# Kernel optimization log

Hardware: AMD Instinct MI355X
Metric: run time of the kernel (lower is better)

The kernel has to match this reference:

```python
import jax, jax.numpy as jnp
import numpy as np

B, N_PER_GRAPH = 16, 512          # uniform graphs -> to_dense_batch is a reshape
N_TOKENS = B * N_PER_GRAPH
M = 32                            # neighbors per node
D_MODEL, D_EDGE, H = 256, 128, 8


def _layernorm(x, g, b, eps=1e-5):
    m = jnp.mean(x, axis=-1, keepdims=True)
    v = jnp.mean((x - m) ** 2, axis=-1, keepdims=True)
    return (x - m) * jax.lax.rsqrt(v + eps) * g + b


def _frame_ops():
    # 2^3 = 8 sign-flip operations, matches FrameAveraging.create_ops
    d = jnp.array([-1.0, 1.0], dtype=jnp.float32)
    g = jnp.meshgrid(d, d, d, indexing='ij')
    return jnp.stack(g, axis=-1).reshape(8, 3)


def _forward(token_embs, geo_feats, edge_feats, neighbor_indices, neighbor_masks,
             ln_qkv_g, ln_qkv_b, W_qkv, b_qkv, ln_e_g, ln_e_b, W_qkv_e, b_qkv_e,
             w_attn, w_edge, W_gate, b_gate, W_fc1, b_fc1, ln_h_g, ln_h_b,
             W_fc2, b_fc2, W_fa, b_fa):
    n = token_embs.shape[0]
    d_head = D_MODEL // H
    de_head = D_EDGE // H
    # qkv transformation
    qkv = _layernorm(token_embs, ln_qkv_g, ln_qkv_b) @ W_qkv + b_qkv
    q, k, v = [a.reshape(n, H, d_head) for a in jnp.split(qkv, 3, axis=-1)]
    qkve = _layernorm(edge_feats, ln_e_g, ln_e_b) @ W_qkv_e + b_qkv_e
    qe, ve = [a.reshape(n, M, H, de_head) for a in jnp.split(qkve, 2, axis=-1)]
    gate = jax.nn.sigmoid(token_embs @ W_gate + b_gate)            # [n,1]
    # GAT-style MLP attention over gathered neighbors
    message = q[:, None] + k[neighbor_indices]                     # [n,M,H,d]
    attn = jnp.einsum('nmhd,d->nmh', message, w_attn) \
         + jnp.einsum('nmhe,e->nmh', qe, w_edge)
    attn = jnp.where(neighbor_masks[..., None], attn, -1e9)
    attn = jax.nn.softmax(jnp.transpose(attn, (0, 2, 1)), axis=-1)  # [n,H,M]
    # context aggregation
    v_n = v[neighbor_indices]                                      # [n,M,H,d]
    scalar_ctx = jnp.einsum('nhm,nmhd->nhd', attn, v_n).reshape(n, -1)
    edge_ctx = jnp.einsum('nhm,nmhd->nhd', attn, ve).reshape(n, -1)
    hcat = jnp.concatenate([scalar_ctx, edge_ctx], axis=-1)
    hmid = _layernorm(jax.nn.gelu(hcat @ W_fc1 + b_fc1, approximate=False), ln_h_g, ln_h_b)
    scalar_out = hmid @ W_fc2 + b_fc2 + token_embs
    # geometric branch with frame averaging (n_heads > 1 path)
    Xb = geo_feats.reshape(B, N_PER_GRAPH, 3)                      # dense batch, full mask
    center = Xb.mean(axis=1)                                       # [B,3]
    Xc = Xb - center[:, None]
    C = jax.lax.stop_gradient(jnp.einsum('bni,bnj->bij', Xc, Xc))  # backward=False -> detach
    _, V = jnp.linalg.eigh(C)                                      # symmetric, UPLO irrelevant
    ops = _frame_ops()
    F_ops = jax.lax.stop_gradient(ops[None, :, None, :] * V[:, None])  # [B,8,3,3]
    h_fr = jnp.einsum('bpj,boji->bopi', Xc, F_ops)                 # [B,8,N,3]
    geo_f = jnp.transpose(h_fr, (1, 0, 2, 3)).reshape(8, n, 3)     # frame-major, node order b*N+p
    geo_neigh = geo_f[:, neighbor_indices]                         # [8,n,M,3]
    geo_ctx = jnp.einsum('nhm,fnmd->fnhd', attn, geo_neigh)        # [8,n,H,3]
    agg = jax.nn.silu(jnp.einsum('fnhd,h->fnd', geo_ctx, W_fa) + b_fa)  # W_frame_agg
    geo_b = jnp.transpose(agg, (1, 0, 2)).reshape(B, N_PER_GRAPH, 8, 3)
    geo_b = jnp.transpose(geo_b, (0, 2, 1, 3))                     # [B,8,N,3]
    inv = jnp.einsum('boij,bopj->bopi', F_ops, geo_b).mean(axis=1) + center[:, None]
    geo_context = inv.reshape(n, 3)
    geo_out = geo_context * gate + geo_feats * (1.0 - gate)
    return scalar_out, geo_out


def setup_inputs() -> dict:
    key = jax.random.key(0)
    ks = jax.random.split(key, 16)
    r = lambda k, shape, s=0.02: (jax.random.normal(k, shape) * s).astype(jnp.float32)
    token_embs = jax.random.normal(ks[0], (N_TOKENS, D_MODEL), dtype=jnp.float32)
    geo_feats = jax.random.normal(ks[1], (N_TOKENS, 3), dtype=jnp.float32)
    edge_feats = jax.random.normal(ks[2], (N_TOKENS, M, D_EDGE), dtype=jnp.float32)
    base = (jnp.arange(N_TOKENS) // N_PER_GRAPH) * N_PER_GRAPH
    neighbor_indices = base[:, None] + jax.random.randint(ks[3], (N_TOKENS, M), 0, N_PER_GRAPH)
    batch_idx = jnp.arange(N_TOKENS) // N_PER_GRAPH
    neighbor_masks = jax.random.uniform(ks[4], (N_TOKENS, M)) < 0.9
    d_head, de_head = D_MODEL // H, D_EDGE // H
    return dict(
        token_embs=token_embs, geo_feats=geo_feats, edge_feats=edge_feats,
        neighbor_indices=neighbor_indices, batch_idx=batch_idx, neighbor_masks=neighbor_masks,
        ln_qkv_g=jnp.ones(D_MODEL), ln_qkv_b=jnp.zeros(D_MODEL),
        W_qkv=r(ks[5], (D_MODEL, 3 * D_MODEL)), b_qkv=jnp.zeros(3 * D_MODEL),
        ln_e_g=jnp.ones(D_EDGE), ln_e_b=jnp.zeros(D_EDGE),
        W_qkv_e=r(ks[6], (D_EDGE, 2 * D_EDGE)), b_qkv_e=jnp.zeros(2 * D_EDGE),
        w_attn=r(ks[7], (d_head,), 0.1), w_edge=r(ks[8], (de_head,), 0.1),
        W_gate=jnp.zeros((D_MODEL, 1)), b_gate=jnp.ones((1,)),   # _init_params
        W_fc1=r(ks[9], (D_MODEL + D_EDGE, D_MODEL)), b_fc1=jnp.zeros(D_MODEL),
        ln_h_g=jnp.ones(D_MODEL), ln_h_b=jnp.zeros(D_MODEL),
        W_fc2=r(ks[10], (D_MODEL, D_MODEL)), b_fc2=jnp.zeros(D_MODEL),
        W_fa=r(ks[11], (H,), 0.3), b_fa=jnp.zeros((1,)),
    )


def reference(token_embs, geo_feats, edge_feats, neighbor_indices, batch_idx, neighbor_masks,
              ln_qkv_g, ln_qkv_b, W_qkv, b_qkv, ln_e_g, ln_e_b, W_qkv_e, b_qkv_e,
              w_attn, w_edge, W_gate, b_gate, W_fc1, b_fc1, ln_h_g, ln_h_b,
              W_fc2, b_fc2, W_fa, b_fa):
    # batch_idx is uniform (arange // N_PER_GRAPH); dense batching handled by reshape
    return _forward(token_embs, geo_feats, edge_feats, neighbor_indices, neighbor_masks,
                    ln_qkv_g, ln_qkv_b, W_qkv, b_qkv, ln_e_g, ln_e_b, W_qkv_e, b_qkv_e,
                    w_attn, w_edge, W_gate, b_gate, W_fc1, b_fc1, ln_h_g, ln_h_b,
                    W_fc2, b_fc2, W_fa, b_fa)
```

## Files before the change

kernel.cpp:

```cpp
#include <hip/hip_runtime.h>
#include <math.h>

#define NTOK 8192
#define NPG  512
#define MNEI 32
#define DM   256
#define DE   128
#define NH   8

#define OFF_WQAK  65536u
#define OFF_BCAT  69632u
#define OFF_WEF   69904u
#define OFF_FLAG  70936u
#define OFF_QA    70944u
#define OFF_KA    136480u
#define OFF_GATE  202016u
#define OFF_VW    210208u
#define OFF_PROJ  2307360u
#define OFF_VMAT  2331936u
#define OFF_CEN   2332080u
#define OFF_HCAT  2332128u

#define OUT_GEO_OFF 2097152

__device__ __forceinline__ void fma4x4(const float4 a, const float4 w, float4* acc) {
    acc[0].x += a.x*w.x; acc[0].y += a.x*w.y; acc[0].z += a.x*w.z; acc[0].w += a.x*w.w;
    acc[1].x += a.y*w.x; acc[1].y += a.y*w.y; acc[1].z += a.y*w.z; acc[1].w += a.y*w.w;
    acc[2].x += a.z*w.x; acc[2].y += a.z*w.y; acc[2].z += a.z*w.z; acc[2].w += a.z*w.w;
    acc[3].x += a.w*w.x; acc[3].y += a.w*w.y; acc[3].z += a.w*w.z; acc[3].w += a.w*w.w;
}

__device__ __forceinline__ float dot4(const float4 a, const float4 b) {
    return a.x*b.x + a.y*b.y + a.z*b.z + a.w*b.w;
}

__global__ __launch_bounds__(256) void k_pre(
    const float* __restrict__ Wqkv, const float* __restrict__ bqkv,
    const float* __restrict__ Wqkve, const float* __restrict__ bqkve,
    const float* __restrict__ w_attn, const float* __restrict__ w_edge,
    const float* __restrict__ lneg, const float* __restrict__ lneb,
    const int* __restrict__ maskp, const float* __restrict__ geo,
    float* __restrict__ ws)
{
    int t = threadIdx.x;
    int b = blockIdx.x;

    if (b == 0) {
        __shared__ int sbad, sflt;
        if (t == 0) { sbad = 0; sflt = 0; }
        __syncthreads();
        int bad = 0, flt = 0;
        for (int i = 0; i < 256; i++) {
            unsigned int w = (unsigned int)maskp[i*256 + t];
            if (w > 1u) bad = 1;
            if (w == 0x3F800000u) flt = 1;
        }
        if (bad) atomicOr(&sbad, 1);
        if (flt) atomicOr(&sflt, 1);
        __syncthreads();
        if (t == 0) {
            int f = sflt ? 2 : (sbad ? 1 : 0);
            ((int*)(ws + OFF_FLAG))[0] = f;
        }
        return;
    }
    if (b == 1) {
        int h = t >> 5, l = t & 31;
        float p = 0.f;
        for (int q = 0; q < 4; q++) {
            int r = l + 32*q;
            float wef = 0.f;
            for (int e = 0; e < 16; e++) wef += Wqkve[r*256 + h*16 + e] * w_edge[e];
            p += lneb[r] * wef;
        }
        for (int m = 16; m >= 1; m >>= 1) p += __shfl_xor(p, m, 32);
        if (l == 0) {
            float s = p;
            for (int d = 0; d < 32; d++) s += bqkv[h*32 + d] * w_attn[d];
            for (int e = 0; e < 16; e++) s += bqkve[h*16 + e] * w_edge[e];
            ws[OFF_BCAT + h] = s;
        }
        if (l == 1) {
            float s = 0.f;
            for (int d = 0; d < 32; d++) s += bqkv[256 + h*32 + d] * w_attn[d];
            ws[OFF_BCAT + 8 + h] = s;
        }
        return;
    }
    if (b < 18) {
        int c = b - 2, k = t;
        int h = c & 7; int off = (c < 8) ? 0 : 256;
        float s = 0.f;
        for (int d = 0; d < 32; d++) s += Wqkv[k*768 + off + h*32 + d] * w_attn[d];
        ws[OFF_WQAK + c*256 + k] = s;
        return;
    }
    if (b < 22) {
        int i = (b - 18)*256 + t;
        int h = i >> 7, r = i & 127;
        float s = 0.f;
        for (int e = 0; e < 16; e++) s += Wqkve[r*256 + h*16 + e] * w_edge[e];
        ws[OFF_WEF + i] = s * lneg[r];
        return;
    }

    {
        __shared__ float sred[4 * 9];
        __shared__ float sres[9];
        __shared__ float sV[9];
        int g = b - 22;
        int wave = t >> 6, lane = t & 63;
        const float* gp = geo + (size_t)g * NPG * 3;

        float x0[2], y0[2], z0[2];
        float sx = 0.f, sy = 0.f, sz = 0.f;
        for (int i = 0; i < 2; i++) {
            int p = t + 256 * i;
            x0[i] = gp[p*3 + 0]; y0[i] = gp[p*3 + 1]; z0[i] = gp[p*3 + 2];
            sx += x0[i]; sy += y0[i]; sz += z0[i];
        }
        {
            float vals[3] = {sx, sy, sz};
            for (int q = 0; q < 3; q++) {
                float v = vals[q];
                for (int m = 32; m >= 1; m >>= 1) v += __shfl_xor(v, m, 64);
                if (lane == 0) sred[wave*9 + q] = v;
            }
        }
        __syncthreads();
        if (t < 3) {
            float s = 0.f;
            for (int w = 0; w < 4; w++) s += sred[w*9 + t];
            sres[t] = s * (1.0f / 512.0f);
        }
        __syncthreads();
        float cx = sres[0], cy = sres[1], cz = sres[2];

        float c6[6] = {0.f, 0.f, 0.f, 0.f, 0.f, 0.f};
        for (int i = 0; i < 2; i++) {
            float dx = x0[i] - cx, dy = y0[i] - cy, dz = z0[i] - cz;
            c6[0] += dx*dx; c6[1] += dx*dy; c6[2] += dx*dz;
            c6[3] += dy*dy; c6[4] += dy*dz; c6[5] += dz*dz;
        }
        for (int q = 0; q < 6; q++) {
            float v = c6[q];
            for (int m = 32; m >= 1; m >>= 1) v += __shfl_xor(v, m, 64);
            if (lane == 0) sred[wave*9 + q] = v;
        }
        __syncthreads();
        if (t < 6) {
            float s = 0.f;
            for (int w = 0; w < 4; w++) s += sred[w*9 + t];
            sres[t] = s;
        }
        __syncthreads();

        if (t == 0) {
            double a[3][3];
            a[0][0] = sres[0]; a[0][1] = a[1][0] = sres[1]; a[0][2] = a[2][0] = sres[2];
            a[1][1] = sres[3]; a[1][2] = a[2][1] = sres[4]; a[2][2] = sres[5];
            double v[3][3] = {{1,0,0},{0,1,0},{0,0,1}};
            const int ps[3] = {0, 0, 1}, qs[3] = {1, 2, 2};
            for (int sweep = 0; sweep < 10; sweep++) {
                for (int pi = 0; pi < 3; pi++) {
                    int p = ps[pi], q = qs[pi];
                    double apq = a[p][q];
                    if (fabs(apq) < 1e-300) continue;
                    double theta = (a[q][q] - a[p][p]) / (2.0 * apq);
                    double tt = ((theta >= 0.0) ? 1.0 : -1.0) / (fabs(theta) + sqrt(theta*theta + 1.0));
                    double c = 1.0 / sqrt(tt*tt + 1.0), s = tt * c;
                    int k = 3 - p - q;
                    double app = a[p][p], aqq = a[q][q], akp = a[k][p], akq = a[k][q];
                    a[p][p] = app - tt * apq;
                    a[q][q] = aqq + tt * apq;
                    a[p][q] = 0.0; a[q][p] = 0.0;
                    a[k][p] = c*akp - s*akq; a[p][k] = a[k][p];
                    a[k][q] = s*akp + c*akq; a[q][k] = a[k][q];
                    for (int kk = 0; kk < 3; kk++) {
                        double vp = v[kk][p], vq = v[kk][q];
                        v[kk][p] = c*vp - s*vq;
                        v[kk][q] = s*vp + c*vq;
                    }
                }
            }
            for (int r = 0; r < 3; r++)
                for (int c2 = 0; c2 < 3; c2++) {
                    float fv = (float)v[r][c2];
                    sV[r*3 + c2] = fv;
                    ws[OFF_VMAT + g*9 + r*3 + c2] = fv;
                }
            ws[OFF_CEN + g*3 + 0] = cx;
            ws[OFF_CEN + g*3 + 1] = cy;
            ws[OFF_CEN + g*3 + 2] = cz;
        }
        __syncthreads();

        for (int i = 0; i < 2; i++) {
            int p = t + 256 * i;
            float dx = x0[i] - cx, dy = y0[i] - cy, dz = z0[i] - cz;
            for (int c = 0; c < 3; c++) {
                float pr = dx * sV[0*3 + c] + dy * sV[1*3 + c] + dz * sV[2*3 + c];
                ws[OFF_PROJ + (size_t)(g*NPG + p)*3 + c] = pr;
            }
        }
    }
}

__global__ __launch_bounds__(256) void k_tokprep(
    const float* __restrict__ tok, const float* __restrict__ ln_g,
    const float* __restrict__ ln_b, const float* __restrict__ Wgate,
    const float* __restrict__ bgate, const float* __restrict__ Wqkv,
    const float* __restrict__ bqkv, float* __restrict__ ws)
{
    __shared__ __align__(16) float sln[256 * 12];
    int t = threadIdx.x;
    int tok0 = blockIdx.x * 8;

    #pragma unroll
    for (int q = 0; q < 8; q++)
        sln[t*12 + q] = tok[(size_t)(tok0 + q) * 256 + t];
    __syncthreads();

    int wave = t >> 6, lane = t & 63;
    for (int rr = 0; rr < 2; rr++) {
        int tt = wave * 2 + rr;
        float s = 0.f, gdot = 0.f;
        float xs[4];
        #pragma unroll
        for (int q = 0; q < 4; q++) {
            int k = lane + 64*q;
            float x = sln[k*12 + tt];
            xs[q] = x; s += x; gdot += x * Wgate[k];
        }
        for (int m = 32; m >= 1; m >>= 1) { s += __shfl_xor(s,m,64); gdot += __shfl_xor(gdot,m,64); }
        float mu = s * (1.0f/256.0f);
        float vs = 0.f;
        #pragma unroll
        for (int q = 0; q < 4; q++) { float d = xs[q]-mu; vs += d*d; }
        for (int m = 32; m >= 1; m >>= 1) vs += __shfl_xor(vs,m,64);
        float rinv = rsqrtf(vs*(1.0f/256.0f)+1e-5f);
        #pragma unroll
        for (int q = 0; q < 4; q++) {
            int k = lane + 64*q;
            sln[k*12 + tt] = (xs[q]-mu)*rinv*ln_g[k] + ln_b[k];
        }
        if (lane == 0) ws[OFF_GATE + tok0 + tt] = 1.0f/(1.0f+expf(-(gdot + bgate[0])));
    }
    __syncthreads();

    {
        int i = t >> 6, j = t & 63;
        const float* Wc = Wqkv + 512 + 4*j;
        float4 acc0 = make_float4(0.f,0.f,0.f,0.f);
        float4 acc1 = make_float4(0.f,0.f,0.f,0.f);
        #pragma unroll 8
        for (int k = 0; k < 256; k++) {
            float a0 = sln[k*12 + 2*i];
            float a1 = sln[k*12 + 2*i + 1];
            float4 w4 = *(const float4*)&Wc[(size_t)k*768];
            acc0.x += a0*w4.x; acc0.y += a0*w4.y; acc0.z += a0*w4.z; acc0.w += a0*w4.w;
            acc1.x += a1*w4.x; acc1.y += a1*w4.y; acc1.z += a1*w4.z; acc1.w += a1*w4.w;
        }
        float4 b4 = *(const float4*)&bqkv[512 + 4*j];
        int n0 = tok0 + 2*i;
        acc0.x += b4.x; acc0.y += b4.y; acc0.z += b4.z; acc0.w += b4.w;
        acc1.x += b4.x; acc1.y += b4.y; acc1.z += b4.z; acc1.w += b4.w;
        *(float4*)&ws[OFF_VW + (size_t)n0*256 + 4*j]     = acc0;
        *(float4*)&ws[OFF_VW + (size_t)(n0+1)*256 + 4*j] = acc1;
    }

    if (t < 128) {
        int col = t & 15, tp = t >> 4;
        const float* wq = ws + OFF_WQAK + col*256;
        float acc = 0.f;
        #pragma unroll 8
        for (int k4 = 0; k4 < 64; k4++) {
            float4 w4 = *(const float4*)&wq[4*k4];
            acc += w4.x * sln[(4*k4+0)*12 + tp]
                 + w4.y * sln[(4*k4+1)*12 + tp]
                 + w4.z * sln[(4*k4+2)*12 + tp]
                 + w4.w * sln[(4*k4+3)*12 + tp];
        }
        acc += ws[OFF_BCAT + col];
        int n = tok0 + tp;
        if (col < 8) ws[OFF_QA + n*8 + col] = acc;
        else         ws[OFF_KA + n*8 + (col - 8)] = acc;
    }
}

__global__ __launch_bounds__(256) void k_attn(
    const float* __restrict__ edge, const int* __restrict__ nbr,
    const void* __restrict__ maskp,
    const float* __restrict__ lneg, const float* __restrict__ lneb,
    const float* __restrict__ bqkve, const float* __restrict__ Wqkve,
    const float* __restrict__ Wfa, const float* __restrict__ bfa,
    const float* __restrict__ geo, float* __restrict__ ws, float* __restrict__ out)
{
    __shared__ __align__(16) float se[32 * 132];
    __shared__ __align__(16) float uSWE[8 * 132];
    __shared__ __align__(16) float sattn[8 * 36];
    __shared__ float srinv[32];
    __shared__ int   snbr[32];
    __shared__ float sg3[4];

    int t = threadIdx.x;
    int n = blockIdx.x;
    int g = n >> 9;
    int flag = ((const int*)(ws + OFF_FLAG))[0];

    int m = t >> 3, sub = t & 7;

    const float4* xp = (const float4*)(edge + (size_t)n * 4096 + m*128 + sub*16);
    float4 x0 = xp[0], x1 = xp[1], x2 = xp[2], x3 = xp[3];

    int nb = nbr[n*32 + m];
    float qa = ws[OFF_QA + n*8 + sub];
    float ka = ws[OFF_KA + (size_t)nb*8 + sub];
    int mv;
    if (flag == 1)      mv = (int)((const unsigned char*)maskp)[n*32 + m];
    else if (flag == 2) mv = (((const float*)maskp)[n*32 + m] != 0.0f) ? 1 : 0;
    else                mv = ((const int*)maskp)[n*32 + m];

    {
        int idx = t * 4;
        int h = idx >> 7, r = idx & 127;
        int s2 = r >> 4, c = r & 15;
        *(float4*)&uSWE[s2*132 + h*16 + c] = *(const float4*)&ws[OFF_WEF + idx];
    }
    if (t < 32) snbr[t] = nbr[n*32 + t];
    __syncthreads();

    {
        float s = x0.x+x0.y+x0.z+x0.w + x1.x+x1.y+x1.z+x1.w
                + x2.x+x2.y+x2.z+x2.w + x3.x+x3.y+x3.z+x3.w;
        for (int mm = 4; mm >= 1; mm >>= 1) s += __shfl_xor(s, mm, 8);
        float mu = s * (1.0f / 128.0f);
        x0.x-=mu; x0.y-=mu; x0.z-=mu; x0.w-=mu;
        x1.x-=mu; x1.y-=mu; x1.z-=mu; x1.w-=mu;
        x2.x-=mu; x2.y-=mu; x2.z-=mu; x2.w-=mu;
        x3.x-=mu; x3.y-=mu; x3.z-=mu; x3.w-=mu;
        float vs = dot4(x0,x0) + dot4(x1,x1) + dot4(x2,x2) + dot4(x3,x3);
        for (int mm = 4; mm >= 1; mm >>= 1) vs += __shfl_xor(vs, mm, 8);
        float rinv = rsqrtf(vs * (1.0f / 128.0f) + 1e-5f);
        float4* sp = (float4*)&se[m*132 + sub*16];
        sp[0] = x0; sp[1] = x1; sp[2] = x2; sp[3] = x3;
        if (sub == 0) srinv[m] = rinv;

        float accl[8];
        const float* wb = &uSWE[sub*132];
        #pragma unroll
        for (int h = 0; h < 8; h++) {
            const float4* wp = (const float4*)(wb + h*16);
            accl[h] = dot4(x0,wp[0]) + dot4(x1,wp[1]) + dot4(x2,wp[2]) + dot4(x3,wp[3]);
        }
        #pragma unroll
        for (int st = 1; st < 8; st <<= 1) {
            #pragma unroll
            for (int h = 0; h < 8; h++) accl[h] += __shfl_xor(accl[h], st, 8);
        }
        float myacc = accl[0];
        #pragma unroll
        for (int h = 1; h < 8; h++) myacc = (sub == h) ? accl[h] : myacc;

        float lg = myacc * rinv + qa + ka;
        if (!mv) lg = -1e9f;
        sattn[sub*36 + m] = lg;
    }
    __syncthreads();

    {
        int h = t >> 5, m2 = t & 31;
        float x = sattn[h*36 + m2];
        float mx = x;
        for (int mm = 16; mm >= 1; mm >>= 1) mx = fmaxf(mx, __shfl_xor(mx, mm, 32));
        float e = expf(x - mx);
        float sum = e;
        for (int mm = 16; mm >= 1; mm >>= 1) sum += __shfl_xor(sum, mm, 32);
        sattn[h*36 + m2] = e / sum;
    }
    __syncthreads();

    float* sew = uSWE;

    int wave = t >> 6;
    if (wave == 0) {
        int c4 = t, h = c4 >> 3;
        const float* vw = ws + OFF_VW;
        float4 acc = make_float4(0.f,0.f,0.f,0.f);
        #pragma unroll 4
        for (int mi = 0; mi < 32; mi++) {
            float a = sattn[h*36 + mi];
            int row = snbr[mi];
            float4 v4 = *(const float4*)&vw[(size_t)row*256 + 4*c4];
            acc.x += a*v4.x; acc.y += a*v4.y; acc.z += a*v4.z; acc.w += a*v4.w;
        }
        *(float4*)&ws[OFF_HCAT + (size_t)n*384 + 4*c4] = acc;
    } else if (wave == 1) {
        int lm = t - 64;
        if (lm < 32) {
            float wmv = 0.f;
            #pragma unroll
            for (int h2 = 0; h2 < 8; h2++) wmv += Wfa[h2] * sattn[h2*36 + lm];
            int row = snbr[lm];
            const float* pp = ws + OFF_PROJ + (size_t)row*3;
            float q0 = wmv * pp[0], q1 = wmv * pp[1], q2 = wmv * pp[2];
            for (int st = 16; st >= 1; st >>= 1) {
                q0 += __shfl_xor(q0, st, 32);
                q1 += __shfl_xor(q1, st, 32);
                q2 += __shfl_xor(q2, st, 32);
            }
            if (lm < 3) {
                float sd = (lm == 0) ? q0 : (lm == 1) ? q1 : q2;
                float bb = bfa[0];
                float p1 = sd + bb, p2 = -sd + bb;
                float s1v = p1 / (1.0f + expf(-p1));
                float s2v = p2 / (1.0f + expf(-p2));
                sg3[lm] = 0.5f * (s1v - s2v);
            }
        }
    } else {
        int rq = t & 31, hb = (t >> 5) & 3;
        float4 e1 = make_float4(0.f,0.f,0.f,0.f);
        float4 e2 = make_float4(0.f,0.f,0.f,0.f);
        #pragma unroll 4
        for (int mi = 0; mi < 32; mi++) {
            float ri = srinv[mi];
            float a1 = sattn[hb*36 + mi] * ri;
            float a2 = sattn[(hb+4)*36 + mi] * ri;
            float4 x4 = *(const float4*)&se[mi*132 + 4*rq];
            e1.x += a1*x4.x; e1.y += a1*x4.y; e1.z += a1*x4.z; e1.w += a1*x4.w;
            e2.x += a2*x4.x; e2.y += a2*x4.y; e2.z += a2*x4.z; e2.w += a2*x4.w;
        }
        float4 g4 = *(const float4*)&lneg[4*rq];
        float4 b4 = *(const float4*)&lneb[4*rq];
        float4 o1, o2;
        o1.x = g4.x*e1.x + b4.x; o1.y = g4.y*e1.y + b4.y;
        o1.z = g4.z*e1.z + b4.z; o1.w = g4.w*e1.w + b4.w;
        o2.x = g4.x*e2.x + b4.x; o2.y = g4.y*e2.y + b4.y;
        o2.z = g4.z*e2.z + b4.z; o2.w = g4.w*e2.w + b4.w;
        *(float4*)&sew[hb*132 + 4*rq]     = o1;
        *(float4*)&sew[(hb+4)*132 + 4*rq] = o2;
    }
    __syncthreads();

    float* sec = se;
    {
        int col4 = t & 31, rgrp = t >> 5;
        int h2 = col4 >> 2;
        const float* wqb = Wqkve + 128 + 4*col4;
        float4 accE = make_float4(0.f,0.f,0.f,0.f);
        #pragma unroll 4
        for (int ri = 0; ri < 16; ri++) {
            int r = rgrp*16 + ri;
            float sv = sew[h2*132 + r];
            float4 w4 = *(const float4*)&wqb[(size_t)r*256];
            accE.x += sv*w4.x; accE.y += sv*w4.y; accE.z += sv*w4.z; accE.w += sv*w4.w;
        }
        *(float4*)&sec[rgrp*128 + 4*col4] = accE;
    }
    __syncthreads();

    if (t < 128) {
        float ec = bqkve[128 + t];
        #pragma unroll
        for (int g2 = 0; g2 < 8; g2++) ec += sec[g2*128 + t];
        ws[OFF_HCAT + (size_t)n*384 + 256 + t] = ec;
    }
    if (t < 3) {
        const float* Vm = ws + OFF_VMAT + g*9;
        float gc = Vm[t*3+0]*sg3[0] + Vm[t*3+1]*sg3[1] + Vm[t*3+2]*sg3[2] + ws[OFF_CEN + g*3 + t];
        float gt = ws[OFF_GATE + n];
        out[OUT_GEO_OFF + (size_t)n*3 + t] = gc * gt + geo[(size_t)n*3 + t] * (1.0f - gt);
    }
}

__global__ __launch_bounds__(256) void k_mlp(
    const float* __restrict__ tok, const float* __restrict__ Wfc1,
    const float* __restrict__ bfc1, const float* __restrict__ lnhg,
    const float* __restrict__ lnhb, const float* __restrict__ Wfc2,
    const float* __restrict__ bfc2, const float* __restrict__ ws,
    float* __restrict__ out)
{
    __shared__ __align__(16) float A[384 * 12];
    __shared__ __align__(16) float R[128 * 16];
    int t = threadIdx.x;
    int tok0 = blockIdx.x * 8;
    int i2 = (t >> 6) & 1, kh = t >> 7, j = t & 63;
    const float* hc = ws + OFF_HCAT;

    #pragma unroll
    for (int q = 0; q < 12; q++) {
        int idx = q*256 + t;
        int tt = idx / 384;
        int k  = idx - tt*384;
        A[k*12 + tt] = hc[(size_t)tok0*384 + idx];
    }
    __syncthreads();

    float4 acc1[4];
    acc1[0] = acc1[1] = acc1[2] = acc1[3] = make_float4(0.f,0.f,0.f,0.f);
    {
        const float* wp = Wfc1 + 4*j;
        int kbase = kh * 192;
        #pragma unroll 8
        for (int kk = 0; kk < 192; kk++) {
            int k = kbase + kk;
            float4 a4 = *(const float4*)&A[k*12 + 4*i2];
            float4 w4 = *(const float4*)&wp[(size_t)k*256];
            fma4x4(a4, w4, acc1);
        }
    }
    if (kh == 1) {
        int rowid = t - 128;
        #pragma unroll
        for (int ti = 0; ti < 4; ti++) *(float4*)&R[rowid*16 + ti*4] = acc1[ti];
    }
    __syncthreads();

    float h[4][4];
    if (kh == 0) {
        float4 b4 = *(const float4*)&bfc1[4*j];
        #pragma unroll
        for (int ti = 0; ti < 4; ti++) {
            float4 p = *(const float4*)&R[t*16 + ti*4];
            float xv[4] = {acc1[ti].x + p.x + b4.x, acc1[ti].y + p.y + b4.y,
                           acc1[ti].z + p.z + b4.z, acc1[ti].w + p.w + b4.w};
            #pragma unroll
            for (int c = 0; c < 4; c++) {
                float x = xv[c];
                h[ti][c] = 0.5f * x * (1.0f + erff(x * 0.70710678118654752f));
            }
        }
        float s[4], qv[4];
        #pragma unroll
        for (int ti = 0; ti < 4; ti++) {
            s[ti]  = h[ti][0] + h[ti][1] + h[ti][2] + h[ti][3];
            qv[ti] = h[ti][0]*h[ti][0] + h[ti][1]*h[ti][1] + h[ti][2]*h[ti][2] + h[ti][3]*h[ti][3];
        }
        for (int m = 32; m >= 1; m >>= 1)
            #pragma unroll
            for (int ti = 0; ti < 4; ti++) {
                s[ti]  += __shfl_xor(s[ti], m, 64);
                qv[ti] += __shfl_xor(qv[ti], m, 64);
            }
        float4 g4 = *(const float4*)&lnhg[4*j];
        float4 b42 = *(const float4*)&lnhb[4*j];
        float gg[4] = {g4.x, g4.y, g4.z, g4.w};
        float bb[4] = {b42.x, b42.y, b42.z, b42.w};
        #pragma unroll
        for (int ti = 0; ti < 4; ti++) {
            float mu = s[ti] * (1.0f/256.0f);
            float var = qv[ti] * (1.0f/256.0f) - mu*mu;
            float rinv = rsqrtf(var + 1e-5f);
            #pragma unroll
            for (int c = 0; c < 4; c++) {
                float hn = (h[ti][c] - mu) * rinv * gg[c] + bb[c];
                A[(4*j + c)*12 + 4*i2 + ti] = hn;
            }
        }
    }
    __syncthreads();

    float4 acc2[4];
    acc2[0] = acc2[1] = acc2[2] = acc2[3] = make_float4(0.f,0.f,0.f,0.f);
    {
        const float* wp = Wfc2 + 4*j;
        int kbase = kh * 128;
        #pragma unroll 8
        for (int kk = 0; kk < 128; kk++) {
            int k = kbase + kk;
            float4 a4 = *(const float4*)&A[k*12 + 4*i2];
            float4 w4 = *(const float4*)&wp[(size_t)k*256];
            fma4x4(a4, w4, acc2);
        }
    }
    if (kh == 1) {
        int rowid = t - 128;
        #pragma unroll
        for (int ti = 0; ti < 4; ti++) *(float4*)&R[rowid*16 + ti*4] = acc2[ti];
    }
    __syncthreads();

    if (kh == 0) {
        float4 b4 = *(const float4*)&bfc2[4*j];
        #pragma unroll
        for (int ti = 0; ti < 4; ti++) {
            float4 p = *(const float4*)&R[t*16 + ti*4];
            size_t o = (size_t)(tok0 + 4*i2 + ti) * 256 + 4*j;
            float4 r4 = *(const float4*)&tok[o];
            float4 v;
            v.x = acc2[ti].x + p.x + b4.x + r4.x;
            v.y = acc2[ti].y + p.y + b4.y + r4.y;
            v.z = acc2[ti].z + p.z + b4.z + r4.z;
            v.w = acc2[ti].w + p.w + b4.w + r4.w;
            *(float4*)&out[o] = v;
        }
    }
}

extern "C" void kernel_launch(void* const* d_in, const int* in_sizes, int n_in,
                              void* d_out, int out_size, void* d_ws, size_t ws_size,
                              hipStream_t stream) {
    (void)in_sizes; (void)n_in; (void)out_size; (void)ws_size;
    const float* tok   = (const float*)d_in[0];
    const float* geo   = (const float*)d_in[1];
    const float* edge  = (const float*)d_in[2];
    const int*   nbr   = (const int*)d_in[3];
    const void*  maskp = d_in[5];
    const float* ln_qkv_g = (const float*)d_in[6];
    const float* ln_qkv_b = (const float*)d_in[7];
    const float* Wqkv  = (const float*)d_in[8];
    const float* bqkv  = (const float*)d_in[9];
    const float* ln_e_g = (const float*)d_in[10];
    const float* ln_e_b = (const float*)d_in[11];
    const float* Wqkve = (const float*)d_in[12];
    const float* bqkve = (const float*)d_in[13];
    const float* w_attn = (const float*)d_in[14];
    const float* w_edge = (const float*)d_in[15];
    const float* Wgate = (const float*)d_in[16];
    const float* bgate = (const float*)d_in[17];
    const float* Wfc1  = (const float*)d_in[18];
    const float* bfc1  = (const float*)d_in[19];
    const float* lnhg  = (const float*)d_in[20];
    const float* lnhb  = (const float*)d_in[21];
    const float* Wfc2  = (const float*)d_in[22];
    const float* bfc2  = (const float*)d_in[23];
    const float* Wfa   = (const float*)d_in[24];
    const float* bfa   = (const float*)d_in[25];
    float* ws  = (float*)d_ws;
    float* out = (float*)d_out;

    k_pre<<<dim3(38), dim3(256), 0, stream>>>(Wqkv, bqkv, Wqkve, bqkve, w_attn, w_edge,
                                              ln_e_g, ln_e_b, (const int*)maskp, geo, ws);
    k_tokprep<<<dim3(1024), dim3(256), 0, stream>>>(tok, ln_qkv_g, ln_qkv_b, Wgate, bgate,
                                                    Wqkv, bqkv, ws);
    k_attn<<<dim3(8192), dim3(256), 0, stream>>>(edge, nbr, maskp, ln_e_g, ln_e_b, bqkve,
                                                 Wqkve, Wfa, bfa, geo, ws, out);
    k_mlp<<<dim3(1024), dim3(256), 0, stream>>>(tok, Wfc1, bfc1, lnhg, lnhb, Wfc2, bfc2, ws, out);
}
```

Baseline: 397.7 us.

## Store edge tile in fp16 shared memory and raise k_attn occupancy

```diff
diff --git a/kernel.cpp b/kernel.cpp
--- a/kernel.cpp
+++ b/kernel.cpp
@@ -1,4 +1,5 @@
 #include <hip/hip_runtime.h>
+#include <hip/hip_fp16.h>
 #include <math.h>
 
 #define NTOK 8192
@@ -288,7 +289,7 @@
     }
 }
 
-__global__ __launch_bounds__(256) void k_attn(
+__global__ __launch_bounds__(256, 8) void k_attn(
     const float* __restrict__ edge, const int* __restrict__ nbr,
     const void* __restrict__ maskp,
     const float* __restrict__ lneg, const float* __restrict__ lneb,
@@ -296,7 +297,7 @@
     const float* __restrict__ Wfa, const float* __restrict__ bfa,
     const float* __restrict__ geo, float* __restrict__ ws, float* __restrict__ out)
 {
-    __shared__ __align__(16) float se[32 * 132];
+    __shared__ __align__(16) unsigned short seh[32 * 136];
     __shared__ __align__(16) float uSWE[8 * 132];
     __shared__ __align__(16) float sattn[8 * 36];
     __shared__ float srinv[32];
@@ -312,15 +313,6 @@
 
     const float4* xp = (const float4*)(edge + (size_t)n * 4096 + m*128 + sub*16);
     float4 x0 = xp[0], x1 = xp[1], x2 = xp[2], x3 = xp[3];
-
-    int nb = nbr[n*32 + m];
-    float qa = ws[OFF_QA + n*8 + sub];
-    float ka = ws[OFF_KA + (size_t)nb*8 + sub];
-    int mv;
-    if (flag == 1)      mv = (int)((const unsigned char*)maskp)[n*32 + m];
-    else if (flag == 2) mv = (((const float*)maskp)[n*32 + m] != 0.0f) ? 1 : 0;
-    else                mv = ((const int*)maskp)[n*32 + m];
-
     {
         int idx = t * 4;
         int h = idx >> 7, r = idx & 127;
@@ -342,8 +334,22 @@
         float vs = dot4(x0,x0) + dot4(x1,x1) + dot4(x2,x2) + dot4(x3,x3);
         for (int mm = 4; mm >= 1; mm >>= 1) vs += __shfl_xor(vs, mm, 8);
         float rinv = rsqrtf(vs * (1.0f / 128.0f) + 1e-5f);
-        float4* sp = (float4*)&se[m*132 + sub*16];
-        sp[0] = x0; sp[1] = x1; sp[2] = x2; sp[3] = x3;
+
+        unsigned int u[8];
+        {
+            __half2 hh;
+            hh = __floats2half2_rn(x0.x, x0.y); u[0] = *(unsigned int*)&hh;
+            hh = __floats2half2_rn(x0.z, x0.w); u[1] = *(unsigned int*)&hh;
+            hh = __floats2half2_rn(x1.x, x1.y); u[2] = *(unsigned int*)&hh;
+            hh = __floats2half2_rn(x1.z, x1.w); u[3] = *(unsigned int*)&hh;
+            hh = __floats2half2_rn(x2.x, x2.y); u[4] = *(unsigned int*)&hh;
+            hh = __floats2half2_rn(x2.z, x2.w); u[5] = *(unsigned int*)&hh;
+            hh = __floats2half2_rn(x3.x, x3.y); u[6] = *(unsigned int*)&hh;
+            hh = __floats2half2_rn(x3.z, x3.w); u[7] = *(unsigned int*)&hh;
+        }
+        uint4* sp = (uint4*)&seh[m*136 + sub*16];
+        sp[0] = make_uint4(u[0], u[1], u[2], u[3]);
+        sp[1] = make_uint4(u[4], u[5], u[6], u[7]);
         if (sub == 0) srinv[m] = rinv;
 
         float accl[8];
@@ -362,7 +368,14 @@
         #pragma unroll
         for (int h = 1; h < 8; h++) myacc = (sub == h) ? accl[h] : myacc;
 
-        float lg = myacc * rinv + qa + ka;
+        int mv;
+        if (flag == 1)      mv = (int)((const unsigned char*)maskp)[n*32 + m];
+        else if (flag == 2) mv = (((const float*)maskp)[n*32 + m] != 0.0f) ? 1 : 0;
+        else                mv = ((const int*)maskp)[n*32 + m];
+
+        float lg = myacc * rinv
+                 + ws[OFF_QA + n*8 + sub]
+                 + ws[OFF_KA + (size_t)snbr[m]*8 + sub];
         if (!mv) lg = -1e9f;
         sattn[sub*36 + m] = lg;
     }
@@ -419,31 +432,36 @@
             }
         }
     } else {
-        int rq = t & 31, hb = (t >> 5) & 3;
-        float4 e1 = make_float4(0.f,0.f,0.f,0.f);
-        float4 e2 = make_float4(0.f,0.f,0.f,0.f);
+        int idx = t - 128;
+        int rh = idx & 15, h = idx >> 4;
+        float4 fA = make_float4(0.f,0.f,0.f,0.f);
+        float4 fB = make_float4(0.f,0.f,0.f,0.f);
         #pragma unroll 4
         for (int mi = 0; mi < 32; mi++) {
-            float ri = srinv[mi];
-            float a1 = sattn[hb*36 + mi] * ri;
-            float a2 = sattn[(hb+4)*36 + mi] * ri;
-            float4 x4 = *(const float4*)&se[mi*132 + 4*rq];
-            e1.x += a1*x4.x; e1.y += a1*x4.y; e1.z += a1*x4.z; e1.w += a1*x4.w;
-            e2.x += a2*x4.x; e2.y += a2*x4.y; e2.z += a2*x4.z; e2.w += a2*x4.w;
-        }
-        float4 g4 = *(const float4*)&lneg[4*rq];
-        float4 b4 = *(const float4*)&lneb[4*rq];
+            float a = sattn[h*36 + mi] * srinv[mi];
+            uint4 v = *(const uint4*)&seh[mi*136 + rh*8];
+            float2 f0 = __half22float2(*(__half2*)&v.x);
+            float2 f1 = __half22float2(*(__half2*)&v.y);
+            float2 f2 = __half22float2(*(__half2*)&v.z);
+            float2 f3 = __half22float2(*(__half2*)&v.w);
+            fA.x += a*f0.x; fA.y += a*f0.y; fA.z += a*f1.x; fA.w += a*f1.y;
+            fB.x += a*f2.x; fB.y += a*f2.y; fB.z += a*f3.x; fB.w += a*f3.y;
+        }
+        float4 g4a = *(const float4*)&lneg[8*rh];
+        float4 g4b = *(const float4*)&lneg[8*rh + 4];
+        float4 b4a = *(const float4*)&lneb[8*rh];
+        float4 b4b = *(const float4*)&lneb[8*rh + 4];
         float4 o1, o2;
-        o1.x = g4.x*e1.x + b4.x; o1.y = g4.y*e1.y + b4.y;
-        o1.z = g4.z*e1.z + b4.z; o1.w = g4.w*e1.w + b4.w;
-        o2.x = g4.x*e2.x + b4.x; o2.y = g4.y*e2.y + b4.y;
-        o2.z = g4.z*e2.z + b4.z; o2.w = g4.w*e2.w + b4.w;
-        *(float4*)&sew[hb*132 + 4*rq]     = o1;
-        *(float4*)&sew[(hb+4)*132 + 4*rq] = o2;
-    }
-    __syncthreads();
-
-    float* sec = se;
+        o1.x = g4a.x*fA.x + b4a.x; o1.y = g4a.y*fA.y + b4a.y;
+        o1.z = g4a.z*fA.z + b4a.z; o1.w = g4a.w*fA.w + b4a.w;
+        o2.x = g4b.x*fB.x + b4b.x; o2.y = g4b.y*fB.y + b4b.y;
+        o2.z = g4b.z*fB.z + b4b.z; o2.w = g4b.w*fB.w + b4b.w;
+        *(float4*)&sew[h*132 + 8*rh]     = o1;
+        *(float4*)&sew[h*132 + 8*rh + 4] = o2;
+    }
+    __syncthreads();
+
+    float* sec = (float*)seh;
     {
         int col4 = t & 31, rgrp = t >> 5;
         int h2 = col4 >> 2;
```

New measurement: 392.2 us. Within noise of the previous version (-1.4%).
